# Optimization experiments

Hardware: AMD Instinct MI355X
Metric: run time of the kernel (lower is better)

The kernel has to match this reference:

```python
import jax, jax.numpy as jnp
import numpy as np

N_NODES = 50000


def _gin_aggregate(x, src, dst):
    # sum_{j in N(i)} x_j via scatter-add over edges; eps=0 so add self term
    msg = x[src]  # [E, d]
    return x + jax.ops.segment_sum(msg, dst, num_segments=N_NODES)


def _mlp(h, Wa, ba, Wb, bb):
    return jax.nn.relu(h @ Wa + ba) @ Wb + bb


def setup_inputs() -> dict:
    key = jax.random.key(0)
    ks = jax.random.split(key, 12)
    d_in, d_h, n_cls, n_edges = 128, 128, 40, 800000
    x = jax.random.normal(ks[0], (N_NODES, d_in), dtype=jnp.float32)
    edge_index = jax.random.randint(ks[1], (2, n_edges), 0, N_NODES, dtype=jnp.int64)
    s = lambda k, sh: jax.random.normal(k, sh, dtype=jnp.float32) / np.sqrt(sh[0])
    return {
        "x": x,
        "edge_index": edge_index,
        "W11": s(ks[2], (d_in, 2 * d_h)), "b11": jnp.zeros((2 * d_h,), jnp.float32),
        "W12": s(ks[3], (2 * d_h, d_h)), "b12": jnp.zeros((d_h,), jnp.float32),
        "W21": s(ks[4], (d_h, 2 * d_h)), "b21": jnp.zeros((2 * d_h,), jnp.float32),
        "W22": s(ks[5], (2 * d_h, d_h)), "b22": jnp.zeros((d_h,), jnp.float32),
        "Wfc": s(ks[6], (d_h, n_cls)), "bfc": jnp.zeros((n_cls,), jnp.float32),
    }


def reference(x, edge_index, W11, b11, W12, b12, W21, b21, W22, b22, Wfc, bfc):
    src, dst = edge_index[0], edge_index[1]
    # GINConv 1: aggregate then MLP, followed by ReLU
    h = _mlp(_gin_aggregate(x, src, dst), W11, b11, W12, b12)
    h = jax.nn.relu(h)
    # GINConv 2
    h = _mlp(_gin_aggregate(h, src, dst), W21, b21, W22, b22)
    h = jax.nn.relu(h)
    # final classifier
    return h @ Wfc + bfc
```

## Files before the change

### kernel.cpp

```cpp
#include <hip/hip_runtime.h>

#define N_NODES 50000
#define N_EDGES 800000
#define NBUCK   98
#define EPB     2048
#define NSB     391
#define BCAP    64
#define CAPB    12288

typedef __attribute__((ext_vector_type(8))) short short8;
typedef __attribute__((ext_vector_type(4))) float floatx4;

__device__ __forceinline__ float b2f(unsigned short u) {
    union { unsigned int i; float f; } v;
    v.i = ((unsigned int)u) << 16;
    return v.f;
}
__device__ __forceinline__ float ubits(unsigned int b) {
    union { unsigned int i; float f; } v;
    v.i = b;
    return v.f;
}
__device__ __forceinline__ unsigned short f2b(float f) {
    union { float f; unsigned int i; } v;
    v.f = f;
    unsigned int r = v.i + 0x7FFFu + ((v.i >> 16) & 1u);
    return (unsigned short)(r >> 16);
}

__global__ __launch_bounds__(256) void prep_scatter(
    const float* __restrict__ x,
    const float* __restrict__ W11, const float* __restrict__ W12,
    const float* __restrict__ W21, const float* __restrict__ W22,
    const float* __restrict__ Wfc,
    const int* __restrict__ srcv, const int* __restrict__ dstv,
    unsigned short* __restrict__ xb,
    unsigned short* __restrict__ Wt11, unsigned short* __restrict__ Wt12,
    unsigned short* __restrict__ Wt21, unsigned short* __restrict__ Wt22,
    unsigned short* __restrict__ Wfct,
    int* __restrict__ cnt, int* __restrict__ tmp) {
    const int bid = blockIdx.x;
    const int tid = threadIdx.x;
    if (bid < NSB) {
        __shared__ int hist[NBUCK];
        const int k = bid;
        const int e0 = k * EPB;
        for (int i = tid; i < NBUCK; i += 256) hist[i] = 0;
        __syncthreads();
#pragma unroll
        for (int j = 0; j < EPB / 256; ++j) {
            int e = e0 + j * 256 + tid;
            if (e < N_EDGES) atomicAdd(&hist[dstv[e] >> 9], 1);
        }
        __syncthreads();
        for (int i = tid; i < NBUCK; i += 256) {
            cnt[i * NSB + k] = hist[i];
            hist[i] = 0;
        }
        __syncthreads();
#pragma unroll
        for (int j = 0; j < EPB / 256; ++j) {
            int e = e0 + j * 256 + tid;
            if (e < N_EDGES) {
                int d = dstv[e];
                int b = d >> 9;
                int r = atomicAdd(&hist[b], 1);
                if (r < BCAP)
                    tmp[((size_t)k * NBUCK + b) * BCAP + r] = srcv[e] | ((d & 511) << 16);
            }
        }
    } else if (bid < NSB + 512) {
        int wb = bid - NSB;
        int which = wb >> 7;
        int idx = (wb & 127) * 256 + tid;
        const float* W = (which == 0) ? W11 : (which == 1) ? W12 : (which == 2) ? W21 : W22;
        unsigned short* Wt = (which == 0) ? Wt11 : (which == 1) ? Wt12 : (which == 2) ? Wt21 : Wt22;
        int K = (which & 1) ? 256 : 128;
        int N = (which & 1) ? 128 : 256;
        int k = idx / N, n = idx - k * N;
        Wt[n * K + k] = f2b(W[idx]);
    } else if (bid < NSB + 536) {
        int idx = (bid - NSB - 512) * 256 + tid;
        int n = idx >> 7, k = idx & 127;
        Wfct[idx] = (n < 40) ? f2b(Wfc[k * 40 + n]) : (unsigned short)0;
    } else {
        int i = (bid - NSB - 536) * 256 + tid;
        const float4 a = *reinterpret_cast<const float4*>(x + (size_t)i * 8);
        const float4 b = *reinterpret_cast<const float4*>(x + (size_t)i * 8 + 4);
        ushort4 u0, u1;
        u0.x = f2b(a.x); u0.y = f2b(a.y); u0.z = f2b(a.z); u0.w = f2b(a.w);
        u1.x = f2b(b.x); u1.y = f2b(b.y); u1.z = f2b(b.z); u1.w = f2b(b.w);
        *reinterpret_cast<ushort4*>(xb + (size_t)i * 8) = u0;
        *reinterpret_cast<ushort4*>(xb + (size_t)i * 8 + 4) = u1;
    }
}

__global__ __launch_bounds__(256) void bucket_sort_ex(const int* __restrict__ cnt,
                                                      const int* __restrict__ tmp,
                                                      int* __restrict__ e_src,
                                                      int* __restrict__ row_ptr) {
    __shared__ int ps[256];
    __shared__ int sb[512];
    __shared__ int sc[512];
    __shared__ int nc[512];
    __shared__ int buf[CAPB];
    const int tid = threadIdx.x;
    const int b = blockIdx.x;

    sc[tid] = (tid < NSB) ? cnt[b * NSB + tid] : 0;
    sc[tid + 256] = (tid + 256 < NSB) ? cnt[b * NSB + tid + 256] : 0;
    __syncthreads();
    const int c0s = sc[2 * tid], c1s = sc[2 * tid + 1];
    ps[tid] = c0s + c1s;
    __syncthreads();
    for (int off = 1; off < 256; off <<= 1) {
        int u = (tid >= off) ? ps[tid - off] : 0;
        __syncthreads();
        ps[tid] += u;
        __syncthreads();
    }
    const int soff0 = ps[tid] - (c0s + c1s);
    sb[2 * tid] = soff0;
    sb[2 * tid + 1] = soff0 + c0s;
    __syncthreads();
    const int S = ps[255];

    const int lane = tid & 63, w = tid >> 6;
    const int hw = w * 2 + (lane >> 5), hl = lane & 31;
    for (int k = hw; k < NSB; k += 8) {
        const int base = sb[k], c = sc[k];
        const int* src = tmp + ((size_t)k * NBUCK + b) * BCAP;
        for (int i = hl; i < c; i += 32)
            if (base + i < CAPB) buf[base + i] = src[i];
    }
    for (int i = tid; i < 512; i += 256) nc[i] = 0;
    __syncthreads();
    for (int e = tid; e < S; e += 256)
        atomicAdd(&nc[(buf[e] >> 16) & 511], 1);
    __syncthreads();

    const int c0 = nc[2 * tid], c1 = nc[2 * tid + 1];
    ps[tid] = c0 + c1;
    __syncthreads();
    for (int off = 1; off < 256; off <<= 1) {
        int u = (tid >= off) ? ps[tid - off] : 0;
        __syncthreads();
        ps[tid] += u;
        __syncthreads();
    }
    const int off0 = ps[tid] - (c0 + c1);
    const int off1 = off0 + c0;
    nc[2 * tid] = off0;
    nc[2 * tid + 1] = off1;
    const int gbase = b * CAPB;
    row_ptr[b * 513 + 2 * tid] = gbase + off0;
    row_ptr[b * 513 + 2 * tid + 1] = gbase + off1;
    if (tid == 0) row_ptr[b * 513 + 512] = gbase + S;
    __syncthreads();

    for (int e = tid; e < S; e += 256) {
        int p = buf[e];
        int dl = (p >> 16) & 511;
        int pos = atomicAdd(&nc[dl], 1);
        e_src[gbase + pos] = p & 0xFFFF;
    }
}

__global__ __launch_bounds__(256) void agg_bf16q(const unsigned short* __restrict__ X,
                                                 const int* __restrict__ row_ptr,
                                                 const int* __restrict__ e_src,
                                                 unsigned short* __restrict__ agg) {
    const int node = (blockIdx.x * 256 + threadIdx.x) >> 6;
    const int lane = threadIdx.x & 63;
    const int qw = lane >> 4, ql = lane & 15;
    const size_t off = (size_t)ql * 8;

    const int rp = node + (node >> 9);
    const int beg = row_ptr[rp], end = row_ptr[rp + 1];
    float acc[8];
#pragma unroll
    for (int k = 0; k < 8; ++k) acc[k] = 0.f;

    if (qw == 0) {
        uint4 u = *reinterpret_cast<const uint4*>(X + (size_t)node * 128 + off);
        const unsigned int* up = (const unsigned int*)&u;
#pragma unroll
        for (int k = 0; k < 4; ++k) {
            acc[2 * k]     += ubits(up[k] << 16);
            acc[2 * k + 1] += ubits(up[k] & 0xFFFF0000u);
        }
    }

    int e = beg + qw;
    for (; e + 12 < end; e += 16) {
        const int s0 = e_src[e], s1 = e_src[e + 4], s2 = e_src[e + 8], s3 = e_src[e + 12];
        uint4 u0 = *reinterpret_cast<const uint4*>(X + (size_t)s0 * 128 + off);
        uint4 u1 = *reinterpret_cast<const uint4*>(X + (size_t)s1 * 128 + off);
        uint4 u2 = *reinterpret_cast<const uint4*>(X + (size_t)s2 * 128 + off);
        uint4 u3 = *reinterpret_cast<const uint4*>(X + (size_t)s3 * 128 + off);
        const unsigned int* p0 = (const unsigned int*)&u0;
        const unsigned int* p1 = (const unsigned int*)&u1;
        const unsigned int* p2 = (const unsigned int*)&u2;
        const unsigned int* p3 = (const unsigned int*)&u3;
#pragma unroll
        for (int k = 0; k < 4; ++k) {
            acc[2 * k]     += ubits(p0[k] << 16) + ubits(p1[k] << 16)
                            + ubits(p2[k] << 16) + ubits(p3[k] << 16);
            acc[2 * k + 1] += ubits(p0[k] & 0xFFFF0000u) + ubits(p1[k] & 0xFFFF0000u)
                            + ubits(p2[k] & 0xFFFF0000u) + ubits(p3[k] & 0xFFFF0000u);
        }
    }
    for (; e + 4 < end; e += 8) {
        const int s0 = e_src[e], s1 = e_src[e + 4];
        uint4 u0 = *reinterpret_cast<const uint4*>(X + (size_t)s0 * 128 + off);
        uint4 u1 = *reinterpret_cast<const uint4*>(X + (size_t)s1 * 128 + off);
        const unsigned int* p0 = (const unsigned int*)&u0;
        const unsigned int* p1 = (const unsigned int*)&u1;
#pragma unroll
        for (int k = 0; k < 4; ++k) {
            acc[2 * k]     += ubits(p0[k] << 16) + ubits(p1[k] << 16);
            acc[2 * k + 1] += ubits(p0[k] & 0xFFFF0000u) + ubits(p1[k] & 0xFFFF0000u);
        }
    }
    if (e < end) {
        const int s = e_src[e];
        uint4 u = *reinterpret_cast<const uint4*>(X + (size_t)s * 128 + off);
        const unsigned int* p = (const unsigned int*)&u;
#pragma unroll
        for (int k = 0; k < 4; ++k) {
            acc[2 * k]     += ubits(p[k] << 16);
            acc[2 * k + 1] += ubits(p[k] & 0xFFFF0000u);
        }
    }

#pragma unroll
    for (int k = 0; k < 8; ++k) acc[k] += __shfl_xor(acc[k], 32);
#pragma unroll
    for (int k = 0; k < 8; ++k) acc[k] += __shfl_xor(acc[k], 16);

    if (qw == 0) {
        ushort4 o0, o1;
        o0.x = f2b(acc[0]); o0.y = f2b(acc[1]); o0.z = f2b(acc[2]); o0.w = f2b(acc[3]);
        o1.x = f2b(acc[4]); o1.y = f2b(acc[5]); o1.z = f2b(acc[6]); o1.w = f2b(acc[7]);
        unsigned short* p = agg + (size_t)node * 128 + off;
        *reinterpret_cast<ushort4*>(p) = o0;
        *reinterpret_cast<ushort4*>(p + 4) = o1;
    }
}

template <bool FUSE>
__global__ __launch_bounds__(256, FUSE ? 2 : 3) void mlp_fused(
    const unsigned short* __restrict__ X, const unsigned short* __restrict__ Wt1,
    const float* __restrict__ b1, const unsigned short* __restrict__ Wt2,
    const float* __restrict__ b2, unsigned short* __restrict__ Y,
    const unsigned short* __restrict__ Wfct, const float* __restrict__ bfc,
    float* __restrict__ out, int M) {
    __shared__ __align__(16) char smem[FUSE ? 57344 : 52224];
    unsigned short* A   = (unsigned short*)smem;
    unsigned short* B2q = (unsigned short*)smem;
    unsigned short* B1h = (unsigned short*)(smem + 17408);
    unsigned short* T   = (unsigned short*)(smem + 17408);
    unsigned short* Hc  = (unsigned short*)(smem + 52224);

    const int tid = threadIdx.x;
    const int m0 = blockIdx.x * 64;
    const int lane = tid & 63, w = tid >> 6;
    const int qm = lane & 15, quad = lane >> 4;

#pragma unroll
    for (int j = 0; j < 4; ++j) {
        int i = j * 256 + tid;
        int r = i >> 4, c8 = (i & 15) << 3;
        uint4 v = {0, 0, 0, 0};
        if (m0 + r < M) v = *reinterpret_cast<const uint4*>(X + (size_t)(m0 + r) * 128 + c8);
        *reinterpret_cast<uint4*>(&A[r * 136 + c8]) = v;
    }

    floatx4 acc1[2][4][2];
#pragma unroll
    for (int c = 0; c < 2; ++c)
#pragma unroll
        for (int mt = 0; mt < 4; ++mt)
#pragma unroll
            for (int nt = 0; nt < 2; ++nt) acc1[c][mt][nt] = {0.f, 0.f, 0.f, 0.f};

    for (int c = 0; c < 2; ++c) {
#pragma unroll
        for (int j = 0; j < 8; ++j) {
            int i = j * 256 + tid;
            int r = i >> 4, c8 = (i & 15) << 3;
            *reinterpret_cast<uint4*>(&B1h[r * 136 + c8]) =
                *reinterpret_cast<const uint4*>(Wt1 + (size_t)(c * 128 + r) * 128 + c8);
        }
        __syncthreads();
#pragma unroll
        for (int ks = 0; ks < 4; ++ks) {
            const int kb = ks * 32 + quad * 8;
            short8 a[4], b[2];
#pragma unroll
            for (int mt = 0; mt < 4; ++mt)
                a[mt] = *reinterpret_cast<const short8*>(&A[(mt * 16 + qm) * 136 + kb]);
#pragma unroll
            for (int nt = 0; nt < 2; ++nt)
                b[nt] = *reinterpret_cast<const short8*>(&B1h[(w * 32 + nt * 16 + qm) * 136 + kb]);
#pragma unroll
            for (int mt = 0; mt < 4; ++mt)
#pragma unroll
                for (int nt = 0; nt < 2; ++nt)
                    acc1[c][mt][nt] = __builtin_amdgcn_mfma_f32_16x16x32_bf16(
                        a[mt], b[nt], acc1[c][mt][nt], 0, 0, 0);
        }
        __syncthreads();
    }

#pragma unroll
    for (int c = 0; c < 2; ++c) {
#pragma unroll
        for (int nt = 0; nt < 2; ++nt) {
            const int jcol = c * 128 + w * 32 + nt * 16 + qm;
            const float bj = b1[jcol];
#pragma unroll
            for (int mt = 0; mt < 4; ++mt)
#pragma unroll
                for (int r = 0; r < 4; ++r)
                    T[(mt * 16 + quad * 4 + r) * 264 + jcol] =
                        f2b(fmaxf(acc1[c][mt][nt][r] + bj, 0.f));
        }
    }

    floatx4 cacc[3];
#pragma unroll
    for (int nt = 0; nt < 3; ++nt) cacc[nt] = {0.f, 0.f, 0.f, 0.f};

    for (int c2 = 0; c2 < 4; ++c2) {
#pragma unroll
        for (int j = 0; j < 4; ++j) {
            int i = j * 256 + tid;
            int r = i >> 5, c8 = (i & 31) << 3;
            *reinterpret_cast<uint4*>(&B2q[r * 264 + c8]) =
                *reinterpret_cast<const uint4*>(Wt2 + (size_t)(c2 * 32 + r) * 256 + c8);
        }
        __syncthreads();

        floatx4 acc2[2];
        acc2[0] = {0.f, 0.f, 0.f, 0.f};
        acc2[1] = {0.f, 0.f, 0.f, 0.f};
#pragma unroll
        for (int ks = 0; ks < 8; ++ks) {
            const int kb = ks * 32 + quad * 8;
            short8 t0 = *reinterpret_cast<const short8*>(&T[((w & 1) * 32 + qm) * 264 + kb]);
            short8 t1 = *reinterpret_cast<const short8*>(&T[((w & 1) * 32 + 16 + qm) * 264 + kb]);
            short8 bb = *reinterpret_cast<const short8*>(&B2q[((w >> 1) * 16 + qm) * 264 + kb]);
            acc2[0] = __builtin_amdgcn_mfma_f32_16x16x32_bf16(t0, bb, acc2[0], 0, 0, 0);
            acc2[1] = __builtin_amdgcn_mfma_f32_16x16x32_bf16(t1, bb, acc2[1], 0, 0, 0);
        }

        const int ncol = c2 * 32 + (w >> 1) * 16 + qm;
        const float bj = b2[ncol];
        if (!FUSE) {
#pragma unroll
            for (int mt2 = 0; mt2 < 2; ++mt2)
#pragma unroll
                for (int r = 0; r < 4; ++r) {
                    int row = m0 + (w & 1) * 32 + mt2 * 16 + quad * 4 + r;
                    if (row < M)
                        Y[(size_t)row * 128 + ncol] = f2b(fmaxf(acc2[mt2][r] + bj, 0.f));
                }
            __syncthreads();
        } else {
            const int lcol = (w >> 1) * 16 + qm;
#pragma unroll
            for (int mt2 = 0; mt2 < 2; ++mt2)
#pragma unroll
                for (int r = 0; r < 4; ++r)
                    Hc[((w & 1) * 32 + mt2 * 16 + quad * 4 + r) * 40 + lcol] =
                        f2b(fmaxf(acc2[mt2][r] + bj, 0.f));
            __syncthreads();
            short8 hf = *reinterpret_cast<const short8*>(&Hc[(w * 16 + qm) * 40 + quad * 8]);
#pragma unroll
            for (int nt = 0; nt < 3; ++nt) {
                short8 bf = *reinterpret_cast<const short8*>(
                    Wfct + (nt * 16 + qm) * 128 + c2 * 32 + quad * 8);
                cacc[nt] = __builtin_amdgcn_mfma_f32_16x16x32_bf16(hf, bf, cacc[nt], 0, 0, 0);
            }
            __syncthreads();
        }
    }

    if (FUSE) {
#pragma unroll
        for (int nt = 0; nt < 3; ++nt) {
            int col = nt * 16 + qm;
            if (col < 40) {
                const float bj = bfc[col];
#pragma unroll
                for (int r = 0; r < 4; ++r) {
                    int row = m0 + w * 16 + quad * 4 + r;
                    if (row < M) out[(size_t)row * 40 + col] = cacc[nt][r] + bj;
                }
            }
        }
    }
}

extern "C" void kernel_launch(void* const* d_in, const int* in_sizes, int n_in,
                              void* d_out, int out_size, void* d_ws, size_t ws_size,
                              hipStream_t stream) {
    const float* x   = (const float*)d_in[0];
    const int*   ei  = (const int*)d_in[1];
    const float* W11 = (const float*)d_in[2];
    const float* b11 = (const float*)d_in[3];
    const float* W12 = (const float*)d_in[4];
    const float* b12 = (const float*)d_in[5];
    const float* W21 = (const float*)d_in[6];
    const float* b21 = (const float*)d_in[7];
    const float* W22 = (const float*)d_in[8];
    const float* b22 = (const float*)d_in[9];
    const float* Wfc = (const float*)d_in[10];
    const float* bfc = (const float*)d_in[11];
    float* out = (float*)d_out;

    const int* srcv = ei;
    const int* dstv = ei + N_EDGES;

    unsigned short* agg  = (unsigned short*)d_ws;
    unsigned short* h    = agg + (size_t)N_NODES * 128;
    unsigned short* xb   = h   + (size_t)N_NODES * 128;
    unsigned short* Wt11 = xb  + (size_t)N_NODES * 128;
    unsigned short* Wt12 = Wt11 + 256 * 128;
    unsigned short* Wt21 = Wt12 + 256 * 128;
    unsigned short* Wt22 = Wt21 + 256 * 128;
    unsigned short* Wfct = Wt22 + 256 * 128;
    int* cnt     = (int*)(Wfct + 48 * 128);
    int* row_ptr = cnt + 38400;
    int* e_src   = row_ptr + 50304;
    int* tmp     = e_src + (size_t)NBUCK * CAPB;

    prep_scatter<<<NSB + 3661, 256, 0, stream>>>(
        x, W11, W12, W21, W22, Wfc, srcv, dstv,
        xb, Wt11, Wt12, Wt21, Wt22, Wfct, cnt, tmp);

    bucket_sort_ex<<<NBUCK, 256, 0, stream>>>(cnt, tmp, e_src, row_ptr);

    const int agg_blocks = N_NODES * 64 / 256;
    const int mlp_blocks = (N_NODES + 63) / 64;

    agg_bf16q<<<agg_blocks, 256, 0, stream>>>(xb, row_ptr, e_src, agg);
    mlp_fused<false><<<mlp_blocks, 256, 0, stream>>>(
        agg, Wt11, b11, Wt12, b12, h, nullptr, nullptr, nullptr, N_NODES);
    agg_bf16q<<<agg_blocks, 256, 0, stream>>>(h, row_ptr, e_src, agg);
    mlp_fused<true><<<mlp_blocks, 256, 0, stream>>>(
        agg, Wt21, b21, Wt22, b22, nullptr, Wfct, bfc, out, N_NODES);
}
```

Baseline: 245.6 us.

## Split each node's edge aggregation across two wavefronts with LDS reduction

The aggregation kernel now assigns two wavefronts (128 threads) per destination node instead of one, so each wave handles half of the edges with a 2-way unrolled loop, and the partial sums are combined through shared memory after a block barrier. The aim is more memory-level parallelism per node and shorter per-wave dependency chains in the gather loop. It doubles the thread count, adds a __syncthreads and an LDS round trip, and wave 0 now writes the output row as ushort2 stores.

New measurement: 258.2 us. +5.1%, slower.

```diff
diff --git a/kernel.cpp b/kernel.cpp
--- a/kernel.cpp
+++ b/kernel.cpp
@@ -166,12 +166,16 @@
     }
 }
 
-__global__ __launch_bounds__(256) void agg_bf16q(const unsigned short* __restrict__ X,
-                                                 const int* __restrict__ row_ptr,
-                                                 const int* __restrict__ e_src,
-                                                 unsigned short* __restrict__ agg) {
-    const int node = (blockIdx.x * 256 + threadIdx.x) >> 6;
-    const int lane = threadIdx.x & 63;
+__global__ __launch_bounds__(256) void agg_bf16q2(const unsigned short* __restrict__ X,
+                                                  const int* __restrict__ row_ptr,
+                                                  const int* __restrict__ e_src,
+                                                  unsigned short* __restrict__ agg) {
+    __shared__ float lbuf[2][2][128];
+    const int tid = threadIdx.x;
+    const int pair = tid >> 7;
+    const int node = blockIdx.x * 2 + pair;
+    const int wv = (tid >> 6) & 1;
+    const int lane = tid & 63;
     const int qw = lane >> 4, ql = lane & 15;
     const size_t off = (size_t)ql * 8;
 
@@ -181,7 +185,7 @@
 #pragma unroll
     for (int k = 0; k < 8; ++k) acc[k] = 0.f;
 
-    if (qw == 0) {
+    if (wv == 0 && qw == 0) {
         uint4 u = *reinterpret_cast<const uint4*>(X + (size_t)node * 128 + off);
         const unsigned int* up = (const unsigned int*)&u;
 #pragma unroll
@@ -191,27 +195,9 @@
         }
     }
 
-    int e = beg + qw;
-    for (; e + 12 < end; e += 16) {
-        const int s0 = e_src[e], s1 = e_src[e + 4], s2 = e_src[e + 8], s3 = e_src[e + 12];
-        uint4 u0 = *reinterpret_cast<const uint4*>(X + (size_t)s0 * 128 + off);
-        uint4 u1 = *reinterpret_cast<const uint4*>(X + (size_t)s1 * 128 + off);
-        uint4 u2 = *reinterpret_cast<const uint4*>(X + (size_t)s2 * 128 + off);
-        uint4 u3 = *reinterpret_cast<const uint4*>(X + (size_t)s3 * 128 + off);
-        const unsigned int* p0 = (const unsigned int*)&u0;
-        const unsigned int* p1 = (const unsigned int*)&u1;
-        const unsigned int* p2 = (const unsigned int*)&u2;
-        const unsigned int* p3 = (const unsigned int*)&u3;
-#pragma unroll
-        for (int k = 0; k < 4; ++k) {
-            acc[2 * k]     += ubits(p0[k] << 16) + ubits(p1[k] << 16)
-                            + ubits(p2[k] << 16) + ubits(p3[k] << 16);
-            acc[2 * k + 1] += ubits(p0[k] & 0xFFFF0000u) + ubits(p1[k] & 0xFFFF0000u)
-                            + ubits(p2[k] & 0xFFFF0000u) + ubits(p3[k] & 0xFFFF0000u);
-        }
-    }
-    for (; e + 4 < end; e += 8) {
-        const int s0 = e_src[e], s1 = e_src[e + 4];
+    int e = beg + wv * 4 + qw;
+    for (; e + 8 < end; e += 16) {
+        const int s0 = e_src[e], s1 = e_src[e + 8];
         uint4 u0 = *reinterpret_cast<const uint4*>(X + (size_t)s0 * 128 + off);
         uint4 u1 = *reinterpret_cast<const uint4*>(X + (size_t)s1 * 128 + off);
         const unsigned int* p0 = (const unsigned int*)&u0;
@@ -239,12 +225,18 @@
     for (int k = 0; k < 8; ++k) acc[k] += __shfl_xor(acc[k], 16);
 
     if (qw == 0) {
-        ushort4 o0, o1;
-        o0.x = f2b(acc[0]); o0.y = f2b(acc[1]); o0.z = f2b(acc[2]); o0.w = f2b(acc[3]);
-        o1.x = f2b(acc[4]); o1.y = f2b(acc[5]); o1.z = f2b(acc[6]); o1.w = f2b(acc[7]);
-        unsigned short* p = agg + (size_t)node * 128 + off;
-        *reinterpret_cast<ushort4*>(p) = o0;
-        *reinterpret_cast<ushort4*>(p + 4) = o1;
+#pragma unroll
+        for (int k = 0; k < 8; ++k) lbuf[pair][wv][ql * 8 + k] = acc[k];
+    }
+    __syncthreads();
+
+    if (wv == 0) {
+        float a0 = lbuf[pair][0][2 * lane] + lbuf[pair][1][2 * lane];
+        float a1 = lbuf[pair][0][2 * lane + 1] + lbuf[pair][1][2 * lane + 1];
+        ushort2 o;
+        o.x = f2b(a0);
+        o.y = f2b(a1);
+        *reinterpret_cast<ushort2*>(agg + (size_t)node * 128 + lane * 2) = o;
     }
 }
 
@@ -442,13 +434,13 @@
 
     bucket_sort_ex<<<NBUCK, 256, 0, stream>>>(cnt, tmp, e_src, row_ptr);
 
-    const int agg_blocks = N_NODES * 64 / 256;
+    const int agg_blocks = N_NODES / 2;
     const int mlp_blocks = (N_NODES + 63) / 64;
 
-    agg_bf16q<<<agg_blocks, 256, 0, stream>>>(xb, row_ptr, e_src, agg);
+    agg_bf16q2<<<agg_blocks, 256, 0, stream>>>(xb, row_ptr, e_src, agg);
     mlp_fused<false><<<mlp_blocks, 256, 0, stream>>>(
         agg, Wt11, b11, Wt12, b12, h, nullptr, nullptr, nullptr, N_NODES);
-    agg_bf16q<<<agg_blocks, 256, 0, stream>>>(h, row_ptr, e_src, agg);
+    agg_bf16q2<<<agg_blocks, 256, 0, stream>>>(h, row_ptr, e_src, agg);
     mlp_fused<true><<<mlp_blocks, 256, 0, stream>>>(
         agg, Wt21, b21, Wt22, b22, nullptr, Wfct, bfc, out, N_NODES);
 }
```

## Prefetch next weight tiles into registers to overlap global loads with MFMA

Applied to the files above, without the earlier changes.

The fused MLP kernel now loads the next chunk of W1 and each next W2 slice from global memory into registers while the current chunk's MFMAs run. It then writes those registers to shared memory after a barrier, instead of doing a blocking global-to-LDS copy at the start of each chunk. This is meant to hide global-load latency behind compute. In exchange it raises register pressure, since the 8 uint4 and 4 uint4 prefetch buffers add to the already large accumulators, which may reduce occupancy.

New measurement: 280.9 us. +14.4%, slower.

```diff
diff --git a/kernel.cpp b/kernel.cpp
--- a/kernel.cpp
+++ b/kernel.cpp
@@ -284,34 +284,71 @@
 #pragma unroll
             for (int nt = 0; nt < 2; ++nt) acc1[c][mt][nt] = {0.f, 0.f, 0.f, 0.f};
 
-    for (int c = 0; c < 2; ++c) {
-#pragma unroll
-        for (int j = 0; j < 8; ++j) {
-            int i = j * 256 + tid;
-            int r = i >> 4, c8 = (i & 15) << 3;
-            *reinterpret_cast<uint4*>(&B1h[r * 136 + c8]) =
-                *reinterpret_cast<const uint4*>(Wt1 + (size_t)(c * 128 + r) * 128 + c8);
-        }
-        __syncthreads();
-#pragma unroll
-        for (int ks = 0; ks < 4; ++ks) {
-            const int kb = ks * 32 + quad * 8;
-            short8 a[4], b[2];
-#pragma unroll
-            for (int mt = 0; mt < 4; ++mt)
-                a[mt] = *reinterpret_cast<const short8*>(&A[(mt * 16 + qm) * 136 + kb]);
+#pragma unroll
+    for (int j = 0; j < 8; ++j) {
+        int i = j * 256 + tid;
+        int r = i >> 4, c8 = (i & 15) << 3;
+        *reinterpret_cast<uint4*>(&B1h[r * 136 + c8]) =
+            *reinterpret_cast<const uint4*>(Wt1 + (size_t)r * 128 + c8);
+    }
+    uint4 wpre[8];
+#pragma unroll
+    for (int j = 0; j < 8; ++j) {
+        int i = j * 256 + tid;
+        int r = i >> 4, c8 = (i & 15) << 3;
+        wpre[j] = *reinterpret_cast<const uint4*>(Wt1 + (size_t)(128 + r) * 128 + c8);
+    }
+    __syncthreads();
+#pragma unroll
+    for (int ks = 0; ks < 4; ++ks) {
+        const int kb = ks * 32 + quad * 8;
+        short8 a[4], b[2];
+#pragma unroll
+        for (int mt = 0; mt < 4; ++mt)
+            a[mt] = *reinterpret_cast<const short8*>(&A[(mt * 16 + qm) * 136 + kb]);
+#pragma unroll
+        for (int nt = 0; nt < 2; ++nt)
+            b[nt] = *reinterpret_cast<const short8*>(&B1h[(w * 32 + nt * 16 + qm) * 136 + kb]);
+#pragma unroll
+        for (int mt = 0; mt < 4; ++mt)
 #pragma unroll
             for (int nt = 0; nt < 2; ++nt)
-                b[nt] = *reinterpret_cast<const short8*>(&B1h[(w * 32 + nt * 16 + qm) * 136 + kb]);
-#pragma unroll
-            for (int mt = 0; mt < 4; ++mt)
-#pragma unroll
-                for (int nt = 0; nt < 2; ++nt)
-                    acc1[c][mt][nt] = __builtin_amdgcn_mfma_f32_16x16x32_bf16(
-                        a[mt], b[nt], acc1[c][mt][nt], 0, 0, 0);
-        }
-        __syncthreads();
-    }
+                acc1[0][mt][nt] = __builtin_amdgcn_mfma_f32_16x16x32_bf16(
+                    a[mt], b[nt], acc1[0][mt][nt], 0, 0, 0);
+    }
+    __syncthreads();
+#pragma unroll
+    for (int j = 0; j < 8; ++j) {
+        int i = j * 256 + tid;
+        int r = i >> 4, c8 = (i & 15) << 3;
+        *reinterpret_cast<uint4*>(&B1h[r * 136 + c8]) = wpre[j];
+    }
+    uint4 bpre[4];
+#pragma unroll
+    for (int j = 0; j < 4; ++j) {
+        int i = j * 256 + tid;
+        int r = i >> 5, c8 = (i & 31) << 3;
+        bpre[j] = *reinterpret_cast<const uint4*>(Wt2 + (size_t)r * 256 + c8);
+    }
+    __syncthreads();
+#pragma unroll
+    for (int ks = 0; ks < 4; ++ks) {
+        const int kb = ks * 32 + quad * 8;
+        short8 a[4], b[2];
+#pragma unroll
+        for (int mt = 0; mt < 4; ++mt)
+            a[mt] = *reinterpret_cast<const short8*>(&A[(mt * 16 + qm) * 136 + kb]);
+#pragma unroll
+        for (int nt = 0; nt < 2; ++nt)
+            b[nt] = *reinterpret_cast<const short8*>(&B1h[(w * 32 + nt * 16 + qm) * 136 + kb]);
+#pragma unroll
+        for (int mt = 0; mt < 4; ++mt)
+#pragma unroll
+            for (int nt = 0; nt < 2; ++nt)
+                acc1[1][mt][nt] = __builtin_amdgcn_mfma_f32_16x16x32_bf16(
+                    a[mt], b[nt], acc1[1][mt][nt], 0, 0, 0);
+    }
+    __syncthreads();
 
 #pragma unroll
     for (int c = 0; c < 2; ++c) {
@@ -327,20 +364,29 @@
                         f2b(fmaxf(acc1[c][mt][nt][r] + bj, 0.f));
         }
     }
+#pragma unroll
+    for (int j = 0; j < 4; ++j) {
+        int i = j * 256 + tid;
+        int r = i >> 5, c8 = (i & 31) << 3;
+        *reinterpret_cast<uint4*>(&B2q[r * 264 + c8]) = bpre[j];
+    }
+    __syncthreads();
 
     floatx4 cacc[3];
 #pragma unroll
     for (int nt = 0; nt < 3; ++nt) cacc[nt] = {0.f, 0.f, 0.f, 0.f};
 
+#pragma unroll
     for (int c2 = 0; c2 < 4; ++c2) {
-#pragma unroll
-        for (int j = 0; j < 4; ++j) {
-            int i = j * 256 + tid;
-            int r = i >> 5, c8 = (i & 31) << 3;
-            *reinterpret_cast<uint4*>(&B2q[r * 264 + c8]) =
-                *reinterpret_cast<const uint4*>(Wt2 + (size_t)(c2 * 32 + r) * 256 + c8);
-        }
-        __syncthreads();
+        if (c2 < 3) {
+#pragma unroll
+            for (int j = 0; j < 4; ++j) {
+                int i = j * 256 + tid;
+                int r = i >> 5, c8 = (i & 31) << 3;
+                bpre[j] = *reinterpret_cast<const uint4*>(
+                    Wt2 + (size_t)((c2 + 1) * 32 + r) * 256 + c8);
+            }
+        }
 
         floatx4 acc2[2];
         acc2[0] = {0.f, 0.f, 0.f, 0.f};
@@ -366,7 +412,16 @@
                     if (row < M)
                         Y[(size_t)row * 128 + ncol] = f2b(fmaxf(acc2[mt2][r] + bj, 0.f));
                 }
-            __syncthreads();
+            if (c2 < 3) {
+                __syncthreads();
+#pragma unroll
+                for (int j = 0; j < 4; ++j) {
+                    int i = j * 256 + tid;
+                    int r = i >> 5, c8 = (i & 31) << 3;
+                    *reinterpret_cast<uint4*>(&B2q[r * 264 + c8]) = bpre[j];
+                }
+                __syncthreads();
+            }
         } else {
             const int lcol = (w >> 1) * 16 + qm;
 #pragma unroll
@@ -382,6 +437,14 @@
                 short8 bf = *reinterpret_cast<const short8*>(
                     Wfct + (nt * 16 + qm) * 128 + c2 * 32 + quad * 8);
                 cacc[nt] = __builtin_amdgcn_mfma_f32_16x16x32_bf16(hf, bf, cacc[nt], 0, 0, 0);
+            }
+            if (c2 < 3) {
+#pragma unroll
+                for (int j = 0; j < 4; ++j) {
+                    int i = j * 256 + tid;
+                    int r = i >> 5, c8 = (i & 31) << 3;
+                    *reinterpret_cast<uint4*>(&B2q[r * 264 + c8]) = bpre[j];
+                }
             }
             __syncthreads();
         }
```
